# Kernel optimization log

Measured on AMD Instinct MI355X. Metric: run time of the kernel, lower is better.

## Reference

```python
import jax, jax.numpy as jnp
import numpy as np

SLOPE = 0.01   # nn.LeakyReLU default negative_slope
EPS = 1e-8     # nn.CosineSimilarity default eps


def leaky_relu(x):
    return jnp.where(x >= 0, x, SLOPE * x)


def node_conv(x, w, P):
    # x: [B,N,F] (N % P == 0), w: [P,F] -> [B, N//P, F]
    B, N, F = x.shape
    xg = x.reshape(B, N // P, P, F)
    return jnp.einsum('bspf,pf->bsf', xg, w)


def attn_pool(x, w, b, P):
    # GraphAttentionPooling: per window of P nodes, softmax(W x + b) over the
    # window, then attention-weighted sum.  x: [B,N,F] -> [B, N//P, F]
    B, N, F = x.shape
    xg = x.reshape(B, N // P, P, F)
    logits = jnp.einsum('bspf,f->bsp', xg, w) + b  # b: [1] broadcasts
    att = jax.nn.softmax(logits, axis=-1)
    return jnp.einsum('bspf,bsp->bsf', xg, att)


def get_adjacent(pooled):
    # Faithful to the original (buggy) triple loop: every off-diagonal entry
    # ends up overwritten by a zero, and A[i,i]=cos(v_i,v_i) only when 2i<S.
    # Then A += I and A <- D^{-1/2} A D^{-1/2} with D = column sums.
    B, S, F = pooled.shape
    nrm = jnp.maximum(jnp.linalg.norm(pooled, axis=-1), EPS)     # [B,S]
    cos_self = jnp.sum(pooled * pooled, axis=-1) / (nrm * nrm)    # [B,S]
    mask = (2 * jnp.arange(S) < S).astype(pooled.dtype)           # [S]
    diag = cos_self * mask + 1.0                                  # + identity
    A = jax.vmap(jnp.diag)(diag)                                  # [B,S,S]
    d = jnp.sum(A, axis=1)                                        # [B,S]
    dinv = 1.0 / jnp.sqrt(d)
    return dinv[:, :, None] * A * dinv[:, None, :]


def setup_inputs() -> dict:
    key = jax.random.key(0)
    ks = jax.random.split(key, 11)
    B, N, F, HID, NCLASS, P = 64, 512, 2048, 1100, 512, 4
    s1 = 1.0 / np.sqrt(F)
    s2 = 1.0 / np.sqrt(HID)
    return {
        'x': jax.random.normal(ks[0], (B, N, F), dtype=jnp.float32),
        'conv1_w': jax.random.uniform(ks[1], (P, F), jnp.float32, -s1, s1),
        'pool1_w': jax.random.uniform(ks[2], (F,), jnp.float32, -s1, s1),
        'pool1_b': jax.random.uniform(ks[3], (1,), jnp.float32, -s1, s1),
        'prop1_W': jax.random.normal(ks[4], (F, HID), jnp.float32) * s1,
        'prop1_B': jax.random.normal(ks[5], (HID,), jnp.float32) * 0.01,
        'conv2_w': jax.random.uniform(ks[6], (P, HID), jnp.float32, -s2, s2),
        'pool2_w': jax.random.uniform(ks[7], (HID,), jnp.float32, -s2, s2),
        'pool2_b': jax.random.uniform(ks[8], (1,), jnp.float32, -s2, s2),
        'prop2_W': jax.random.normal(ks[9], (HID, NCLASS), jnp.float32) * s2,
        'prop2_B': jax.random.normal(ks[10], (NCLASS,), jnp.float32) * 0.01,
        'pooling_size': 4,
    }


def reference(x, conv1_w, pool1_w, pool1_b, prop1_W, prop1_B,
              conv2_w, pool2_w, pool2_b, prop2_W, prop2_B, pooling_size):
    P = pooling_size
    # stage 1
    pooled1 = attn_pool(x, pool1_w, pool1_b, P)      # [B,S,F]
    h = node_conv(x, conv1_w, P)                      # [B,S,F]
    adj1 = get_adjacent(pooled1)                      # [B,S,S]
    h = jnp.einsum('bij,bjf->bif', adj1, h) @ prop1_W + prop1_B
    h = leaky_relu(h)                                 # [B,S,1100]
    # stage 2
    pooled2 = attn_pool(h, pool2_w, pool2_b, P)       # [B,S2,1100]
    h2 = node_conv(h, conv2_w, P)                     # [B,S2,1100]
    adj2 = get_adjacent(pooled2)                      # [B,S2,S2]
    out = jnp.einsum('bij,bjf->bif', adj2, h2) @ prop2_W + prop2_B
    return leaky_relu(out)                            # [B,S2,nclass]
```

## Files before the change

kernel.cpp:

```cpp
#include <hip/hip_runtime.h>
#include <cstdint>
#include <cstddef>


using u16 = unsigned short;
using u32 = unsigned int;
using floatx4 = __attribute__((ext_vector_type(4))) float;
using shortx8 = __attribute__((ext_vector_type(8))) short;

#define OUT_MODE 1

__device__ __forceinline__ float bf_lo(u32 u) { return __uint_as_float(u << 16); }
__device__ __forceinline__ float bf_hi(u32 u) { return __uint_as_float(u & 0xffff0000u); }
__device__ __forceinline__ float bf2f(u16 s) { return __uint_as_float(((u32)s) << 16); }
__device__ __forceinline__ u16 f2bf(float f) {
  u32 u = __float_as_uint(f);
  u += 0x7fffu + ((u >> 16) & 1u);
  return (u16)(u >> 16);
}

__device__ __forceinline__ float ld_elem(const void* b, size_t i, int isf32) {
  return isf32 ? ((const float*)b)[i] : bf2f(((const u16*)b)[i]);
}
__device__ __forceinline__ void ld8(const void* b, size_t i, int isf32, float* o) {
  if (isf32) {
    const float* p = (const float*)b + i;
    float4 a = *(const float4*)p, c = *(const float4*)(p + 4);
    o[0]=a.x; o[1]=a.y; o[2]=a.z; o[3]=a.w; o[4]=c.x; o[5]=c.y; o[6]=c.z; o[7]=c.w;
  } else {
    const u16* p = (const u16*)b + i;
    uint2 a = *(const uint2*)p, c = *(const uint2*)(p + 4);
    o[0]=bf_lo(a.x); o[1]=bf_hi(a.x); o[2]=bf_lo(a.y); o[3]=bf_hi(a.y);
    o[4]=bf_lo(c.x); o[5]=bf_hi(c.x); o[6]=bf_lo(c.y); o[7]=bf_hi(c.y);
  }
}

#define GLDS16(gp, lp) __builtin_amdgcn_global_load_lds( \
    (const __attribute__((address_space(1))) void*)(gp), \
    (__attribute__((address_space(3))) void*)(lp), 16, 0, 0)

__global__ __launch_bounds__(256) void dtype_probe(const u32* __restrict__ x,
                                                   int* __restrict__ flag) {
  __shared__ int cnt[256];
  int t = threadIdx.x, c = 0;
  for (int i = t; i < 1024; i += 256) {
    u32 e = (x[i] >> 7) & 0xFFu;
    c += (e >= 110u && e <= 134u) ? 1 : 0;
  }
  cnt[t] = c;
  __syncthreads();
  for (int s = 128; s > 0; s >>= 1) {
    if (t < s) cnt[t] += cnt[t + s];
    __syncthreads();
  }
  if (t == 0) *flag = (cnt[0] < 512) ? 1 : 0;
}

__global__ __launch_bounds__(256) void transpose2_bf16(
    const void* __restrict__ W1, u16* __restrict__ W1t,
    const void* __restrict__ W2, u16* __restrict__ W2t,
    const int* __restrict__ dflag)
{
  int wf = *dflag;
  __shared__ float tile[64][65];
  int id = blockIdx.x;
  const void* W; u16* Wt; int K, N, Kpad, k0, n0;
  if (id < 576) {
    W = W1; Wt = W1t; K = 2048; N = 1100; Kpad = 2048;
    k0 = (id % 32) * 64; n0 = (id / 32) * 64;
  } else {
    id -= 576;
    W = W2; Wt = W2t; K = 1100; N = 512; Kpad = 1152;
    k0 = (id % 18) * 64; n0 = (id / 18) * 64;
  }
  int t = threadIdx.x;
  int a = t & 63, b4 = t >> 6;
  for (int kk = b4; kk < 64; kk += 4) {
    int gk = k0 + kk, gn = n0 + a;
    tile[kk][a] = (gk < K && gn < N) ? ld_elem(W, (size_t)gk * N + gn, wf) : 0.f;
  }
  __syncthreads();
  for (int nn = b4; nn < 64; nn += 4) {
    Wt[(size_t)(n0 + nn) * Kpad + (size_t)(k0 + a)] = f2bf(tile[a][nn]);
  }
}

__global__ __launch_bounds__(256) void nodeconv_x(
    const void* __restrict__ X, const void* __restrict__ Wc,
    u16* __restrict__ XC, int K, int mbase,
    const int* __restrict__ dflag, int xmode, int wmode)
{
  int fl = (xmode == 2 || wmode == 2) ? *dflag : 0;
  int xf = (xmode == 2) ? fl : xmode;
  int wf = (wmode == 2) ? fl : wmode;
  int m = blockIdx.x, t = threadIdx.x;
  size_t xb = ((size_t)(mbase + m) * 4) * (size_t)K + (size_t)t * 8;
  float a[8] = {0.f, 0.f, 0.f, 0.f, 0.f, 0.f, 0.f, 0.f};
#pragma unroll
  for (int p = 0; p < 4; ++p) {
    float xv[8], wv[8];
    ld8(X, xb + (size_t)p * K, xf, xv);
    ld8(Wc, (size_t)p * K + (size_t)t * 8, wf, wv);
#pragma unroll
    for (int j = 0; j < 8; ++j) a[j] += xv[j] * wv[j];
  }
  u32 o0 = (u32)f2bf(a[0]) | ((u32)f2bf(a[1]) << 16);
  u32 o1 = (u32)f2bf(a[2]) | ((u32)f2bf(a[3]) << 16);
  u32 o2 = (u32)f2bf(a[4]) | ((u32)f2bf(a[5]) << 16);
  u32 o3 = (u32)f2bf(a[6]) | ((u32)f2bf(a[7]) << 16);
  uint4 ov; ov.x = o0; ov.y = o1; ov.z = o2; ov.w = o3;
  *(uint4*)&XC[(size_t)m * K + (size_t)t * 8] = ov;
}

template <int BM, int BN, int WM, int WN, int EPI>
__global__ __launch_bounds__(WM * WN * 64) void gemm_bf16(
    const u16* __restrict__ A, int lda,
    const u16* __restrict__ Bt, int ldb,
    const void* __restrict__ bias, const void* __restrict__ w2,
    void* __restrict__ C, int ldc,
    int Nn, int K, int mout0,
    const int* __restrict__ dflag, int wmode, int of32m)
{
  constexpr int T = WM * WN * 64;
  constexpr int WTM = BM / WM, WTN = BN / WN;
  constexpr int MI = WTM / 16, NI = WTN / 16;
  constexpr int AOC = (BM * 4 + T - 1) / T, BOC = (BN * 4 + T - 1) / T;
  __shared__ alignas(16) u16 As[2][BM * 32];
  __shared__ alignas(16) u16 Bs[2][BN * 32];

  int wf = (wmode == 2) ? *dflag : wmode;
  int tid = threadIdx.x, lane = tid & 63, wave = tid >> 6;

  int nx = gridDim.x, ny = gridDim.y;
  int lin = blockIdx.y * nx + blockIdx.x;
  int nwg = nx * ny;
  int q = nwg >> 3, r = nwg & 7;
  int xcd = lin & 7, wi = lin >> 3;
  int g = (xcd < r ? xcd * (q + 1) : r * (q + 1) + (xcd - r) * q) + wi;
  int bx = g / ny, by = g - bx * ny;

  int m0 = by * BM, n0 = bx * BN;
  int wrow = (wave / WN) * WTM, wcol = (wave % WN) * WTN;
  int quad = lane >> 4, lm = lane & 15;

  const u16* asrc[AOC];
  const u16* bsrc[BOC];
#pragma unroll
  for (int o = 0; o < AOC; ++o) {
    int idx = o * T + tid;
    asrc[o] = (idx < BM * 4)
        ? A + (size_t)(m0 + (idx % BM)) * lda + (idx / BM) * 8 : A;
  }
#pragma unroll
  for (int o = 0; o < BOC; ++o) {
    int idx = o * T + tid;
    bsrc[o] = (idx < BN * 4)
        ? Bt + (size_t)(n0 + (idx % BN)) * ldb + (idx / BN) * 8 : Bt;
  }

  auto STAGE = [&](int buf, int it) {
    int k0 = it << 5;
#pragma unroll
    for (int o = 0; o < AOC; ++o)
      if (o * T + wave * 64 < BM * 4)
        GLDS16(asrc[o] + k0, &As[buf][(o * T + wave * 64) * 8]);
#pragma unroll
    for (int o = 0; o < BOC; ++o)
      if (o * T + wave * 64 < BN * 4)
        GLDS16(bsrc[o] + k0, &Bs[buf][(o * T + wave * 64) * 8]);
  };

  auto COMPUTE = [&](int buf, floatx4 (&acc)[MI][NI]) {
    shortx8 av[MI], bv[NI];
#pragma unroll
    for (int mi = 0; mi < MI; ++mi)
      av[mi] = *(const shortx8*)&As[buf][(size_t)(quad * BM + wrow + mi * 16 + lm) * 8];
#pragma unroll
    for (int ni = 0; ni < NI; ++ni)
      bv[ni] = *(const shortx8*)&Bs[buf][(size_t)(quad * BN + wcol + ni * 16 + lm) * 8];
#pragma unroll
    for (int mi = 0; mi < MI; ++mi)
#pragma unroll
      for (int ni = 0; ni < NI; ++ni)
        acc[mi][ni] = __builtin_amdgcn_mfma_f32_16x16x32_bf16(av[mi], bv[ni], acc[mi][ni], 0, 0, 0);
  };

  floatx4 acc[MI][NI] = {};
  int kiters = K >> 5;

  STAGE(0, 0);
  __syncthreads();

  for (int it = 0; it < kiters - 1; ++it) {
    int cur = it & 1;
    STAGE(cur ^ 1, it + 1);
    COMPUTE(cur, acc);
    __syncthreads();
  }
  COMPUTE((kiters - 1) & 1, acc);

#pragma unroll
  for (int ni = 0; ni < NI; ++ni) {
    int gn = n0 + wcol + ni * 16 + lm;
    float bb = (gn < Nn) ? ld_elem(bias, gn, wf) : 0.f;
    if (EPI == 1) {
      float wv[4];
#pragma unroll
      for (int r = 0; r < 4; ++r)
        wv[r] = (gn < Nn) ? ld_elem(w2, (size_t)r * Nn + gn, wf) : 0.f;
#pragma unroll
      for (int mi = 0; mi < MI; ++mi) {
        float h2 = 0.f;
#pragma unroll
        for (int r = 0; r < 4; ++r) {
          float v = acc[mi][ni][r] + bb;
          v = (v >= 0.f) ? v : 0.01f * v;
          h2 += v * wv[r];
        }
        int s = (mout0 + m0 + wrow + mi * 16 + quad * 4) >> 2;
        ((u16*)C)[(size_t)s * ldc + gn] = f2bf(h2);
      }
    } else {
      if (gn < Nn) {
#pragma unroll
        for (int mi = 0; mi < MI; ++mi) {
#pragma unroll
          for (int r = 0; r < 4; ++r) {
            int gm = mout0 + m0 + wrow + mi * 16 + quad * 4 + r;
            float v = acc[mi][ni][r] + bb;
            v = (v >= 0.f) ? v : 0.01f * v;
            size_t ci = (size_t)gm * ldc + gn;
            if (of32m) ((float*)C)[ci] = v;
            else       ((u16*)C)[ci]   = f2bf(v);
          }
        }
      }
    }
  }
}

extern "C" void kernel_launch(void* const* d_in, const int* in_sizes, int n_in,
                              void* d_out, int out_size, void* d_ws, size_t ws_size,
                              hipStream_t stream) {
  const void* x  = d_in[0];
  const void* w1 = d_in[1];
  const void* W1 = d_in[4];
  const void* b1 = d_in[5];
  const void* w2 = d_in[6];
  const void* W2 = d_in[9];
  const void* b2 = d_in[10];

  char* ws = (char*)d_ws;
  int* dflag = (int*)ws;
  u16* W1t = (u16*)(ws + 256);
  u16* W2t = (u16*)(ws + 256 + 4718592);
  u16* H2  = (u16*)(ws + 256 + 4718592 + 1179648);
  const size_t fixed = 256 + 4718592 + 1179648 + 4718592;
  u16* XC = (u16*)(ws + fixed);

  size_t rem = (ws_size > fixed) ? ws_size - fixed : 0;
  size_t cmax = rem / (2048 * 2);
  int CM = (cmax > 8192) ? 8192 : (int)cmax;
  CM &= ~127;
  if (CM < 128) CM = 128;

  dtype_probe<<<1, 256, 0, stream>>>((const u32*)x, dflag);
  transpose2_bf16<<<720, 256, 0, stream>>>(W1, W1t, W2, W2t, dflag);

  for (int mb = 0; mb < 8192; mb += CM) {
    int cm = 8192 - mb; if (cm > CM) cm = CM;
    nodeconv_x<<<cm, 256, 0, stream>>>(x, w1, XC, 2048, mb, dflag, 2, 2);
    gemm_bf16<128, 128, 2, 4, 1><<<dim3(9, cm / 128), 512, 0, stream>>>(
        XC, 2048, W1t, 2048, b1, w2, H2, 1152, 1100, 2048, mb, dflag, 2, 0);
  }
  gemm_bf16<64, 64, 2, 4, 0><<<dim3(8, 32), 512, 0, stream>>>(
      H2, 1152, W2t, 1152, b2, nullptr, d_out, 512, 512, 1152, 0, dflag, 2, OUT_MODE);
}
```

Baseline: 537.4 us.

## Triple-buffer GEMM LDS stages with explicit vmcnt waits and prefetch distance two

Turns the bf16 MFMA GEMM's double-buffered global_load_lds pipeline into a three-stage ring that prefetches two K-tiles ahead. Before each compute it waits with a hand-written s_waitcnt vmcnt sized to the per-wave load count, rather than relying on __syncthreads draining every load. The aim is to hide more global-memory latency behind MFMA work. In exchange it uses 1.5x the LDS, which may lower occupancy, and adds a second barrier per iteration. The vm_wait helper only handles counts up to 4, so tile configs issuing more loads per stage would skip the wait entirely.

After: 543.7 us. About the same (+1.2%).

```diff
diff --git a/kernel.cpp b/kernel.cpp
--- a/kernel.cpp
+++ b/kernel.cpp
@@ -38,6 +38,17 @@
 #define GLDS16(gp, lp) __builtin_amdgcn_global_load_lds( \
     (const __attribute__((address_space(1))) void*)(gp), \
     (__attribute__((address_space(3))) void*)(lp), 16, 0, 0)
+
+__device__ __forceinline__ void vm_wait(int n) {
+  switch (n) {
+    case 0: asm volatile("s_waitcnt vmcnt(0)" ::: "memory"); break;
+    case 1: asm volatile("s_waitcnt vmcnt(1)" ::: "memory"); break;
+    case 2: asm volatile("s_waitcnt vmcnt(2)" ::: "memory"); break;
+    case 3: asm volatile("s_waitcnt vmcnt(3)" ::: "memory"); break;
+    case 4: asm volatile("s_waitcnt vmcnt(4)" ::: "memory"); break;
+    default: break;
+  }
+}
 
 __global__ __launch_bounds__(256) void dtype_probe(const u32* __restrict__ x,
                                                    int* __restrict__ flag) {
@@ -125,8 +136,8 @@
   constexpr int WTM = BM / WM, WTN = BN / WN;
   constexpr int MI = WTM / 16, NI = WTN / 16;
   constexpr int AOC = (BM * 4 + T - 1) / T, BOC = (BN * 4 + T - 1) / T;
-  __shared__ alignas(16) u16 As[2][BM * 32];
-  __shared__ alignas(16) u16 Bs[2][BN * 32];
+  __shared__ alignas(16) u16 As[3][BM * 32];
+  __shared__ alignas(16) u16 Bs[3][BN * 32];
 
   int wf = (wmode == 2) ? *dflag : wmode;
   int tid = threadIdx.x, lane = tid & 63, wave = tid >> 6;
@@ -158,6 +169,12 @@
         ? Bt + (size_t)(n0 + (idx % BN)) * ldb + (idx / BN) * 8 : Bt;
   }
 
+  int V = 0;
+#pragma unroll
+  for (int o = 0; o < AOC; ++o) if (o * T + wave * 64 < BM * 4) ++V;
+#pragma unroll
+  for (int o = 0; o < BOC; ++o) if (o * T + wave * 64 < BN * 4) ++V;
+
   auto STAGE = [&](int buf, int it) {
     int k0 = it << 5;
 #pragma unroll
@@ -189,15 +206,20 @@
   int kiters = K >> 5;
 
   STAGE(0, 0);
-  __syncthreads();
-
-  for (int it = 0; it < kiters - 1; ++it) {
-    int cur = it & 1;
-    STAGE(cur ^ 1, it + 1);
-    COMPUTE(cur, acc);
-    __syncthreads();
-  }
-  COMPUTE((kiters - 1) & 1, acc);
+  if (kiters > 1) STAGE(1, 1);
+
+  for (int it = 0; it < kiters; ++it) {
+    if (it + 2 < kiters) STAGE((it + 2) % 3, it + 2);
+    int rem = kiters - 1 - it; if (rem > 2) rem = 2;
+    vm_wait(V * rem);
+    __builtin_amdgcn_s_barrier();
+    COMPUTE(it % 3, acc);
+    if (it + 1 < kiters) {
+      asm volatile("s_waitcnt lgkmcnt(0)" ::: "memory");
+      __builtin_amdgcn_sched_barrier(0);
+      __builtin_amdgcn_s_barrier();
+    }
+  }
 
 #pragma unroll
   for (int ni = 0; ni < NI; ++ni) {
```
